# Optimization experiments

Hardware: AMD Instinct MI355X
Metric: run time of the kernel (lower is better)

The kernel has to match this reference:

```python
import jax, jax.numpy as jnp
import numpy as np

DEPTH = 8
IN_FEATURES = 512
OUT_FEATURES = 256
LEAF_COUNT = 2 ** DEPTH          # 256
GATE_COUNT = LEAF_COUNT - 1      # 255
BATCH = 65536


def setup_inputs() -> dict:
    key = jax.random.key(0)
    k1, k2, k3 = jax.random.split(key, 3)
    x = jax.random.normal(k1, (BATCH, IN_FEATURES), dtype=jnp.float32)
    # gw stored transposed as (in_features, gate_count), kaiming-like scale
    gw = jax.random.normal(k2, (IN_FEATURES, GATE_COUNT), dtype=jnp.float32) * (1.0 / np.sqrt(IN_FEATURES))
    gb = jnp.zeros((GATE_COUNT,), dtype=jnp.float32)
    z = jax.random.normal(k3, (OUT_FEATURES, LEAF_COUNT), dtype=jnp.float32)
    return {"x": x, "gw": gw, "gb": gb, "z": z}


def _leaf_probs(x, gw, gb):
    # gatings: (B, gate_count); node it's left child (2p+1) uses g, right child (2p+2) uses 1-g
    g = jax.nn.sigmoid(x @ gw + gb)
    B = x.shape[0]
    dens = jnp.ones((B, 1), dtype=x.dtype)
    for d in range(DEPTH):  # level-wise vectorized traversal, O(depth) steps
        lo, hi = 2 ** d - 1, 2 ** (d + 1) - 1
        gl = g[:, lo:hi]  # (B, 2^d) gatings at this level
        # interleave [parent*g, parent*(1-g)] -> children order matches heap layout
        dens = jnp.stack([dens * gl, dens * (1.0 - gl)], axis=-1).reshape(B, -1)
    return dens  # (B, leaf_count)


def reference(x, gw, gb, z):
    leaf = _leaf_probs(x, gw, gb)        # (B, L)
    # constant projection: z @ leaf_probs^T, then transpose -> (B, out)
    return leaf @ z.T
```

## Files before the change

### kernel.cpp

```cpp
#include <hip/hip_runtime.h>
#include <hip/hip_bf16.h>
#include <stdint.h>


typedef short bf16x8 __attribute__((ext_vector_type(8)));
typedef float f32x4  __attribute__((ext_vector_type(4)));

__device__ __forceinline__ unsigned short f2bf(float f) {
    union { float f; uint32_t u; } c; c.f = f;
    uint32_t u = c.u;
    return (unsigned short)((u + 0x7FFFu + ((u >> 16) & 1u)) >> 16);
}

__device__ __forceinline__ uint32_t pkbf(float a, float b) {
    union { __hip_bfloat162 h; uint32_t u; } cv;
    cv.h = __float22bfloat162_rn(make_float2(a, b));
    return cv.u;
}

__global__ __launch_bounds__(256) void softtree_prep(
    const float* __restrict__ gw, const float* __restrict__ z,
    unsigned short* __restrict__ gwt, unsigned short* __restrict__ zb)
{
    if (blockIdx.x < 32) {
        __shared__ float tsm[64][65];
        const int k0 = (blockIdx.x >> 2) * 64;
        const int n0 = (blockIdx.x & 3) * 64;
        const int r = threadIdx.x >> 6;
        const int c = threadIdx.x & 63;
        const int n = n0 + c;
        #pragma unroll
        for (int i = 0; i < 16; ++i) {
            int kk = r + i * 4;
            tsm[kk][c] = (n < 255) ? gw[(size_t)(k0 + kk) * 255 + n] : 0.0f;
        }
        __syncthreads();
        #pragma unroll
        for (int i = 0; i < 16; ++i) {
            int nn = r + i * 4;
            gwt[(size_t)(n0 + nn) * 512 + k0 + c] = f2bf(tsm[c][nn]);
        }
    } else {
        int base = (blockIdx.x - 32) * 1024 + threadIdx.x * 4;
        const float4 v = *(const float4*)(z + base);
        ushort4 o;
        o.x = f2bf(v.x); o.y = f2bf(v.y); o.z = f2bf(v.z); o.w = f2bf(v.w);
        *(ushort4*)(zb + base) = o;
    }
}

__global__ __launch_bounds__(512, 4) void softtree_g(
    const float* __restrict__ x, const float* __restrict__ gb,
    const unsigned short* __restrict__ gwt, float* __restrict__ g)
{
    __shared__ char smraw[81920];

    const int tid  = threadIdx.x;
    const int lane = tid & 63;
    const int wv   = tid >> 6;
    const int q    = lane >> 4;
    const int l15  = lane & 15;
    const int wr   = wv & 3;
    const int wc   = wv >> 2;
    const int R0   = blockIdx.x * 128;

    float gbv[8];
    #pragma unroll
    for (int nt = 0; nt < 8; ++nt) {
        int col = 128 * wc + nt * 16 + l15;
        gbv[nt] = (col < 255) ? gb[col] : 0.0f;
    }
    asm volatile("s_waitcnt vmcnt(0)" ::: "memory");

    const float* xsrc0 = x + (size_t)(R0 + 16 * wv + (lane >> 3)) * 512
                           + (size_t)(((lane & 7) ^ (lane >> 3)) * 4);
    const unsigned short* gsrc0 = gwt + (size_t)(32 * wv + (lane >> 2)) * 512
                                      + (size_t)(((lane & 3) ^ ((lane >> 2) & 3)) * 8);
    const uint32_t xdst = (uint32_t)wv * 2048;
    const uint32_t gdst = 49152u + (uint32_t)wv * 2048;

    #define ISSUE_X(kc, xb)                                                                    \
        do {                                                                                   \
            const float* s_ = xsrc0 + (kc) * 32;                                               \
            __builtin_amdgcn_global_load_lds(                                                  \
                (const __attribute__((address_space(1))) void*)(s_),                           \
                (__attribute__((address_space(3))) void*)(smraw + (xb) * 16384 + xdst),        \
                16, 0, 0);                                                                     \
            __builtin_amdgcn_global_load_lds(                                                  \
                (const __attribute__((address_space(1))) void*)(s_ + 8 * 512),                 \
                (__attribute__((address_space(3))) void*)(smraw + (xb) * 16384 + xdst + 1024), \
                16, 0, 0);                                                                     \
        } while (0)

    #define ISSUE_G(kc, gwb)                                                                   \
        do {                                                                                   \
            const unsigned short* s_ = gsrc0 + (kc) * 32;                                      \
            __builtin_amdgcn_global_load_lds(                                                  \
                (const __attribute__((address_space(1))) void*)(s_),                           \
                (__attribute__((address_space(3))) void*)(smraw + (gwb) * 16384 + gdst),       \
                16, 0, 0);                                                                     \
            __builtin_amdgcn_global_load_lds(                                                  \
                (const __attribute__((address_space(1))) void*)(s_ + 16 * 512),                \
                (__attribute__((address_space(3))) void*)(smraw + (gwb) * 16384 + gdst + 1024),\
                16, 0, 0);                                                                     \
        } while (0)

    f32x4 acc[2][8];
    #pragma unroll
    for (int t = 0; t < 2; ++t)
        #pragma unroll
        for (int i = 0; i < 8; ++i) acc[t][i] = (f32x4){0.f, 0.f, 0.f, 0.f};

    ISSUE_X(0, 0);
    ISSUE_G(0, 0);
    ISSUE_X(1, 1);

    int xb = 0, gwb = 0;
    for (int kc = 0; kc < 15; ++kc) {
        asm volatile("s_waitcnt vmcnt(2)" ::: "memory");
        __builtin_amdgcn_s_barrier();
        __builtin_amdgcn_sched_barrier(0);

        ISSUE_G(kc + 1, gwb ^ 1);
        if (kc < 14) {
            int xb2 = xb + 2; if (xb2 >= 3) xb2 -= 3;
            ISSUE_X(kc + 2, xb2);
        }

        {
            const char* xbase = smraw + xb * 16384;
            const char* gbase = smraw + 49152 + gwb * 16384;
            bf16x8 a[2];
            #pragma unroll
            for (int t = 0; t < 2; ++t) {
                const char* ra = xbase + (64 * t + 16 * wr + l15) * 128;
                f32x4 lo = *(const f32x4*)(ra + (((2 * q)     ^ (l15 & 7)) * 16));
                f32x4 hi = *(const f32x4*)(ra + (((2 * q + 1) ^ (l15 & 7)) * 16));
                union { bf16x8 v; uint32_t u[4]; } pk;
                pk.u[0] = pkbf(lo[0], lo[1]); pk.u[1] = pkbf(lo[2], lo[3]);
                pk.u[2] = pkbf(hi[0], hi[1]); pk.u[3] = pkbf(hi[2], hi[3]);
                a[t] = pk.v;
            }
            __builtin_amdgcn_s_setprio(1);
            #pragma unroll
            for (int nt = 0; nt < 8; ++nt) {
                const bf16x8 b = *(const bf16x8*)(gbase + (128 * wc + nt * 16 + l15) * 64
                                                        + ((q ^ (l15 & 3)) * 16));
                acc[0][nt] = __builtin_amdgcn_mfma_f32_16x16x32_bf16(a[0], b, acc[0][nt], 0, 0, 0);
                acc[1][nt] = __builtin_amdgcn_mfma_f32_16x16x32_bf16(a[1], b, acc[1][nt], 0, 0, 0);
            }
            __builtin_amdgcn_s_setprio(0);
        }

        xb = (xb == 2) ? 0 : xb + 1;
        gwb ^= 1;
    }

    asm volatile("s_waitcnt vmcnt(0)" ::: "memory");
    __builtin_amdgcn_s_barrier();
    __builtin_amdgcn_sched_barrier(0);
    {
        const char* xbase = smraw + xb * 16384;
        const char* gbase = smraw + 49152 + gwb * 16384;
        bf16x8 a[2];
        #pragma unroll
        for (int t = 0; t < 2; ++t) {
            const char* ra = xbase + (64 * t + 16 * wr + l15) * 128;
            f32x4 lo = *(const f32x4*)(ra + (((2 * q)     ^ (l15 & 7)) * 16));
            f32x4 hi = *(const f32x4*)(ra + (((2 * q + 1) ^ (l15 & 7)) * 16));
            union { bf16x8 v; uint32_t u[4]; } pk;
            pk.u[0] = pkbf(lo[0], lo[1]); pk.u[1] = pkbf(lo[2], lo[3]);
            pk.u[2] = pkbf(hi[0], hi[1]); pk.u[3] = pkbf(hi[2], hi[3]);
            a[t] = pk.v;
        }
        __builtin_amdgcn_s_setprio(1);
        #pragma unroll
        for (int nt = 0; nt < 8; ++nt) {
            const bf16x8 b = *(const bf16x8*)(gbase + (128 * wc + nt * 16 + l15) * 64
                                                    + ((q ^ (l15 & 3)) * 16));
            acc[0][nt] = __builtin_amdgcn_mfma_f32_16x16x32_bf16(a[0], b, acc[0][nt], 0, 0, 0);
            acc[1][nt] = __builtin_amdgcn_mfma_f32_16x16x32_bf16(a[1], b, acc[1][nt], 0, 0, 0);
        }
        __builtin_amdgcn_s_setprio(0);
    }

    #undef ISSUE_X
    #undef ISSUE_G

    #pragma unroll
    for (int t = 0; t < 2; ++t) {
        #pragma unroll
        for (int nt = 0; nt < 8; ++nt) {
            const int col = 128 * wc + nt * 16 + l15;
            #pragma unroll
            for (int r = 0; r < 4; ++r) {
                const int row = R0 + t * 64 + 16 * wr + 4 * q + r;
                float v = acc[t][nt][r] + gbv[nt];
                g[(size_t)row * 256 + col] = 1.0f / (1.0f + __expf(-v));
            }
        }
    }
}

__global__ __launch_bounds__(512, 4) void softtree_tree(
    const float* __restrict__ g, const unsigned short* __restrict__ zb,
    float* __restrict__ out)
{
    __shared__ float gs[64 * 260];

    const int tid  = threadIdx.x;
    const int lane = tid & 63;
    const int wv   = tid >> 6;
    const int q    = lane >> 4;
    const int l15  = lane & 15;
    const int wr   = wv & 3;
    const int wc   = wv >> 2;
    const int R0   = blockIdx.x * 128;

    const int srow = tid >> 3;
    const int scol = (tid & 7) * 32;

    for (int t = 0; t < 2; ++t) {
        if (t) __syncthreads();

        const float* gsrc = g + (size_t)(R0 + 64 * t + srow) * 256 + scol;
        #pragma unroll
        for (int i = 0; i < 8; ++i) {
            f32x4 v = *(const f32x4*)(gsrc + 4 * i);
            *(f32x4*)(gs + srow * 260 + scol + 4 * i) = v;
        }
        __syncthreads();

        const float* gr = gs + (16 * wr + l15) * 260;
        float g0v = gr[0];
        float t1v[2] = { g0v, 1.0f - g0v };
        float t2v[4], t3v[8];
        #pragma unroll
        for (int u = 0; u < 2; ++u) {
            float gl = gr[1 + u];
            t2v[2 * u] = t1v[u] * gl; t2v[2 * u + 1] = t1v[u] - t2v[2 * u];
        }
        #pragma unroll
        for (int u = 0; u < 4; ++u) {
            float gl = gr[3 + u];
            t3v[2 * u] = t2v[u] * gl; t3v[2 * u + 1] = t2v[u] - t3v[2 * u];
        }
        bf16x8 a2[8];
        #pragma unroll
        for (int c = 0; c < 8; ++c) {
            const int G = c * 4 + q;
            float p = t3v[c];
            float g3 = gr[7 + c];
            p = (q & 2) ? (p - p * g3) : (p * g3);
            float g4 = gr[15 + 2 * c + (q >> 1)];
            p = (q & 1) ? (p - p * g4) : (p * g4);
            float g5 = gr[31 + G];
            float a0 = p * g5, a1 = p - a0;
            float g6a = gr[63 + 2 * G], g6b = gr[64 + 2 * G];
            float b00 = a0 * g6a, b01 = a0 - b00;
            float b10 = a1 * g6b, b11 = a1 - b10;
            float g70 = gr[127 + 4 * G], g71 = gr[128 + 4 * G];
            float g72 = gr[129 + 4 * G], g73 = gr[130 + 4 * G];
            float lf0 = b00 * g70, lf1 = b00 - lf0;
            float lf2 = b01 * g71, lf3 = b01 - lf2;
            float lf4 = b10 * g72, lf5 = b10 - lf4;
            float lf6 = b11 * g73, lf7 = b11 - lf6;
            union { bf16x8 v; uint32_t u[4]; } pk;
            pk.u[0] = pkbf(lf0, lf1);
            pk.u[1] = pkbf(lf2, lf3);
            pk.u[2] = pkbf(lf4, lf5);
            pk.u[3] = pkbf(lf6, lf7);
            a2[c] = pk.v;
        }

        f32x4 acc2[8];
        #pragma unroll
        for (int i = 0; i < 8; ++i) acc2[i] = (f32x4){0.f, 0.f, 0.f, 0.f};
        __builtin_amdgcn_s_setprio(1);
        #pragma unroll
        for (int nt = 0; nt < 8; ++nt) {
            const unsigned short* zrow = zb + (size_t)(128 * wc + nt * 16 + l15) * 256 + q * 8;
            #pragma unroll
            for (int c = 0; c < 8; ++c) {
                bf16x8 b = *(const bf16x8*)(zrow + c * 32);
                acc2[nt] = __builtin_amdgcn_mfma_f32_16x16x32_bf16(a2[c], b, acc2[nt], 0, 0, 0);
            }
        }
        __builtin_amdgcn_s_setprio(0);

        #pragma unroll
        for (int nt = 0; nt < 8; ++nt) {
            const int col = 128 * wc + nt * 16 + l15;
            #pragma unroll
            for (int r = 0; r < 4; ++r) {
                const int row = R0 + t * 64 + 16 * wr + 4 * q + r;
                out[(size_t)row * 256 + col] = acc2[nt][r];
            }
        }
    }
}

extern "C" void kernel_launch(void* const* d_in, const int* in_sizes, int n_in,
                              void* d_out, int out_size, void* d_ws, size_t ws_size,
                              hipStream_t stream) {
    const float* x  = (const float*)d_in[0];
    const float* gw = (const float*)d_in[1];
    const float* gb = (const float*)d_in[2];
    const float* z  = (const float*)d_in[3];
    float* outp = (float*)d_out;

    unsigned short* gwt = (unsigned short*)d_ws;
    unsigned short* zbf = gwt + 256 * 512;

    softtree_prep<<<96, 256, 0, stream>>>(gw, z, gwt, zbf);
    softtree_g<<<512, 512, 0, stream>>>(x, gb, gwt, outp);
    softtree_tree<<<512, 512, 0, stream>>>(outp, zbf, outp);
}
```

Before: 300.9 us.

## Split tree kernel into leaf-probability pass and LDS-pipelined output GEMM

The fused tree kernel, which built leaf probabilities and then ran an MFMA GEMM reading z straight from global memory, is split into two kernels. The first writes bf16 leaf probabilities to a workspace buffer. The second runs a GEMM that stages leaf and z tiles into LDS with global_load_lds, using a triple buffer for leaf and a double buffer for z with a swizzle, and overlaps the loads with MFMA. The gating output now goes to its own workspace buffer instead of reusing the output tensor. This adds one more launch and a 32MB bf16 round trip through global memory, in exchange for better operand reuse and latency hiding in the GEMM.

```diff
diff --git a/kernel.cpp b/kernel.cpp
--- a/kernel.cpp
+++ b/kernel.cpp
@@ -202,19 +202,17 @@
     }
 }
 
-__global__ __launch_bounds__(512, 4) void softtree_tree(
-    const float* __restrict__ g, const unsigned short* __restrict__ zb,
-    float* __restrict__ out)
+__global__ __launch_bounds__(512, 4) void softtree_leaf(
+    const float* __restrict__ g, unsigned short* __restrict__ leaf)
 {
     __shared__ float gs[64 * 260];
 
     const int tid  = threadIdx.x;
     const int lane = tid & 63;
-    const int wv   = tid >> 6;
     const int q    = lane >> 4;
     const int l15  = lane & 15;
+    const int wv   = tid >> 6;
     const int wr   = wv & 3;
-    const int wc   = wv >> 2;
     const int R0   = blockIdx.x * 128;
 
     const int srow = tid >> 3;
@@ -232,6 +230,7 @@
         __syncthreads();
 
         const float* gr = gs + (16 * wr + l15) * 260;
+        const int row = R0 + 64 * t + 16 * wr + l15;
         float g0v = gr[0];
         float t1v[2] = { g0v, 1.0f - g0v };
         float t2v[4], t3v[8];
@@ -245,7 +244,6 @@
             float gl = gr[3 + u];
             t3v[2 * u] = t2v[u] * gl; t3v[2 * u + 1] = t2v[u] - t3v[2 * u];
         }
-        bf16x8 a2[8];
         #pragma unroll
         for (int c = 0; c < 8; ++c) {
             const int G = c * 4 + q;
@@ -265,36 +263,136 @@
             float lf2 = b01 * g71, lf3 = b01 - lf2;
             float lf4 = b10 * g72, lf5 = b10 - lf4;
             float lf6 = b11 * g73, lf7 = b11 - lf6;
-            union { bf16x8 v; uint32_t u[4]; } pk;
+            union { uint4 u4; uint32_t u[4]; } pk;
             pk.u[0] = pkbf(lf0, lf1);
             pk.u[1] = pkbf(lf2, lf3);
             pk.u[2] = pkbf(lf4, lf5);
             pk.u[3] = pkbf(lf6, lf7);
-            a2[c] = pk.v;
-        }
-
-        f32x4 acc2[8];
-        #pragma unroll
-        for (int i = 0; i < 8; ++i) acc2[i] = (f32x4){0.f, 0.f, 0.f, 0.f};
+            *(uint4*)(leaf + (size_t)row * 256 + 32 * c + 8 * q) = pk.u4;
+        }
+    }
+}
+
+__global__ __launch_bounds__(512, 4) void softtree_out(
+    const unsigned short* __restrict__ leaf, const unsigned short* __restrict__ zb,
+    float* __restrict__ out)
+{
+    __shared__ char smraw[57344];
+
+    const int tid  = threadIdx.x;
+    const int lane = tid & 63;
+    const int wv   = tid >> 6;
+    const int q    = lane >> 4;
+    const int l15  = lane & 15;
+    const int wr   = wv & 3;
+    const int wc   = wv >> 2;
+    const int R0   = blockIdx.x * 128;
+
+    const unsigned short* lsrc0 = leaf + (size_t)(R0 + 16 * wv + (lane >> 2)) * 256
+                                       + (size_t)(((lane & 3) ^ ((lane >> 2) & 3)) * 8);
+    const unsigned short* zsrc0 = zb + (size_t)(32 * wv + (lane >> 2)) * 256
+                                     + (size_t)(((lane & 3) ^ ((lane >> 2) & 3)) * 8);
+    const uint32_t ldst = (uint32_t)wv * 1024;
+    const uint32_t zdst = 24576u + (uint32_t)wv * 2048;
+
+    #define ISSUE_L(kc, lb_)                                                                   \
+        __builtin_amdgcn_global_load_lds(                                                      \
+            (const __attribute__((address_space(1))) void*)(lsrc0 + (kc) * 32),                \
+            (__attribute__((address_space(3))) void*)(smraw + (lb_) * 8192 + ldst),            \
+            16, 0, 0)
+
+    #define ISSUE_Z(kc, zb_)                                                                   \
+        do {                                                                                   \
+            const unsigned short* s_ = zsrc0 + (kc) * 32;                                      \
+            __builtin_amdgcn_global_load_lds(                                                  \
+                (const __attribute__((address_space(1))) void*)(s_),                           \
+                (__attribute__((address_space(3))) void*)(smraw + (zb_) * 16384 + zdst),       \
+                16, 0, 0);                                                                     \
+            __builtin_amdgcn_global_load_lds(                                                  \
+                (const __attribute__((address_space(1))) void*)(s_ + 4096),                    \
+                (__attribute__((address_space(3))) void*)(smraw + (zb_) * 16384 + zdst + 1024),\
+                16, 0, 0);                                                                     \
+        } while (0)
+
+    f32x4 acc[2][8];
+    #pragma unroll
+    for (int t = 0; t < 2; ++t)
+        #pragma unroll
+        for (int i = 0; i < 8; ++i) acc[t][i] = (f32x4){0.f, 0.f, 0.f, 0.f};
+
+    ISSUE_L(0, 0);
+    ISSUE_Z(0, 0);
+    ISSUE_L(1, 1);
+
+    int lb = 0, zbuf = 0;
+    for (int kc = 0; kc < 7; ++kc) {
+        asm volatile("s_waitcnt vmcnt(1)" ::: "memory");
+        __builtin_amdgcn_s_barrier();
+        __builtin_amdgcn_sched_barrier(0);
+
+        ISSUE_Z(kc + 1, zbuf ^ 1);
+        if (kc < 6) {
+            int lb2 = lb + 2; if (lb2 >= 3) lb2 -= 3;
+            ISSUE_L(kc + 2, lb2);
+        }
+
+        {
+            const char* lbase = smraw + lb * 8192;
+            const char* zbase = smraw + 24576 + zbuf * 16384;
+            bf16x8 a[2];
+            #pragma unroll
+            for (int t = 0; t < 2; ++t)
+                a[t] = *(const bf16x8*)(lbase + (((64 * t + 16 * wr + l15) * 4
+                                                  + (q ^ (l15 & 3))) * 16));
+            __builtin_amdgcn_s_setprio(1);
+            #pragma unroll
+            for (int nt = 0; nt < 8; ++nt) {
+                const int n = 128 * wc + nt * 16 + l15;
+                const bf16x8 b = *(const bf16x8*)(zbase + ((n * 4 + (q ^ (l15 & 3))) * 16));
+                acc[0][nt] = __builtin_amdgcn_mfma_f32_16x16x32_bf16(a[0], b, acc[0][nt], 0, 0, 0);
+                acc[1][nt] = __builtin_amdgcn_mfma_f32_16x16x32_bf16(a[1], b, acc[1][nt], 0, 0, 0);
+            }
+            __builtin_amdgcn_s_setprio(0);
+        }
+
+        lb = (lb == 2) ? 0 : lb + 1;
+        zbuf ^= 1;
+    }
+
+    asm volatile("s_waitcnt vmcnt(0)" ::: "memory");
+    __builtin_amdgcn_s_barrier();
+    __builtin_amdgcn_sched_barrier(0);
+    {
+        const char* lbase = smraw + lb * 8192;
+        const char* zbase = smraw + 24576 + zbuf * 16384;
+        bf16x8 a[2];
+        #pragma unroll
+        for (int t = 0; t < 2; ++t)
+            a[t] = *(const bf16x8*)(lbase + (((64 * t + 16 * wr + l15) * 4
+                                              + (q ^ (l15 & 3))) * 16));
         __builtin_amdgcn_s_setprio(1);
         #pragma unroll
         for (int nt = 0; nt < 8; ++nt) {
-            const unsigned short* zrow = zb + (size_t)(128 * wc + nt * 16 + l15) * 256 + q * 8;
-            #pragma unroll
-            for (int c = 0; c < 8; ++c) {
-                bf16x8 b = *(const bf16x8*)(zrow + c * 32);
-                acc2[nt] = __builtin_amdgcn_mfma_f32_16x16x32_bf16(a2[c], b, acc2[nt], 0, 0, 0);
-            }
+            const int n = 128 * wc + nt * 16 + l15;
+            const bf16x8 b = *(const bf16x8*)(zbase + ((n * 4 + (q ^ (l15 & 3))) * 16));
+            acc[0][nt] = __builtin_amdgcn_mfma_f32_16x16x32_bf16(a[0], b, acc[0][nt], 0, 0, 0);
+            acc[1][nt] = __builtin_amdgcn_mfma_f32_16x16x32_bf16(a[1], b, acc[1][nt], 0, 0, 0);
         }
         __builtin_amdgcn_s_setprio(0);
-
+    }
+
+    #undef ISSUE_L
+    #undef ISSUE_Z
+
+    #pragma unroll
+    for (int t = 0; t < 2; ++t) {
         #pragma unroll
         for (int nt = 0; nt < 8; ++nt) {
             const int col = 128 * wc + nt * 16 + l15;
             #pragma unroll
             for (int r = 0; r < 4; ++r) {
                 const int row = R0 + t * 64 + 16 * wr + 4 * q + r;
-                out[(size_t)row * 256 + col] = acc2[nt][r];
+                out[(size_t)row * 256 + col] = acc[t][nt][r];
             }
         }
     }
@@ -309,10 +407,13 @@
     const float* z  = (const float*)d_in[3];
     float* outp = (float*)d_out;
 
-    unsigned short* gwt = (unsigned short*)d_ws;
-    unsigned short* zbf = gwt + 256 * 512;
+    unsigned short* gwt  = (unsigned short*)d_ws;
+    unsigned short* zbf  = gwt + 256 * 512;
+    float*          gbuf = (float*)((char*)d_ws + (1u << 20));
+    unsigned short* leaf = (unsigned short*)((char*)d_ws + 70u * (1u << 20));
 
     softtree_prep<<<96, 256, 0, stream>>>(gw, z, gwt, zbf);
-    softtree_g<<<512, 512, 0, stream>>>(x, gb, gwt, outp);
-    softtree_tree<<<512, 512, 0, stream>>>(outp, zbf, outp);
-}
+    softtree_g<<<512, 512, 0, stream>>>(x, gb, gwt, gbuf);
+    softtree_leaf<<<512, 512, 0, stream>>>(gbuf, leaf);
+    softtree_out<<<512, 512, 0, stream>>>(leaf, zbf, outp);
+}
```

Result: faster. 275.5 us (-8.4%).
